# Optimization experiments

Hardware: AMD Instinct MI355X
Metric: run time of the kernel (lower is better)

Reference implementation:

```python
import jax, jax.numpy as jnp
import numpy as np

N_NODES = 100000
N_EDGES = 1000000
D = 64            # node_hidden
IN_DIM = 4 * D    # 256
MLP_H = 32
EPS = 1e-5


def setup_inputs() -> dict:
    key = jax.random.key(0)
    ks = jax.random.split(key, 6)
    h = jax.random.normal(ks[0], (N_NODES, D), dtype=jnp.float32)
    edge_pairs = jax.random.randint(ks[1], (2, N_EDGES), 0, N_NODES, dtype=jnp.int64)
    # LayerNorm params
    gamma = jnp.ones((IN_DIM,), dtype=jnp.float32)
    beta = jnp.zeros((IN_DIM,), dtype=jnp.float32)
    # MLP params (PyTorch Linear default init: U(-1/sqrt(fan_in), 1/sqrt(fan_in)))
    b1_bound = 1.0 / np.sqrt(IN_DIM)
    W1 = jax.random.uniform(ks[2], (IN_DIM, MLP_H), minval=-b1_bound, maxval=b1_bound, dtype=jnp.float32)
    b1 = jax.random.uniform(ks[3], (MLP_H,), minval=-b1_bound, maxval=b1_bound, dtype=jnp.float32)
    b2_bound = 1.0 / np.sqrt(MLP_H)
    W2 = jax.random.uniform(ks[4], (MLP_H, 1), minval=-b2_bound, maxval=b2_bound, dtype=jnp.float32)
    b2 = jax.random.uniform(ks[5], (1,), minval=-b2_bound, maxval=b2_bound, dtype=jnp.float32)
    return {"h": h, "edge_pairs": edge_pairs, "gamma": gamma, "beta": beta,
            "W1": W1, "b1": b1, "W2": W2, "b2": b2}


def reference(h, edge_pairs, gamma, beta, W1, b1, W2, b2):
    u = h[edge_pairs[0]]                                    # [E, D]
    v = h[edge_pairs[1]]                                    # [E, D]
    feat = jnp.concatenate([u, v, jnp.abs(u - v), u * v], axis=-1)  # [E, 4D]
    mu = jnp.mean(feat, axis=-1, keepdims=True)
    var = jnp.mean(jnp.square(feat - mu), axis=-1, keepdims=True)
    feat = (feat - mu) * jax.lax.rsqrt(var + EPS) * gamma + beta
    hmid = jax.nn.relu(feat @ W1 + b1)                      # [E, MLP_H]; dropout inactive at eval
    logit = hmid @ W2 + b2                                  # [E, 1]
    return logit.reshape(-1)
```

## Files before the change

kernel.cpp:

```cpp
#include <hip/hip_runtime.h>

#define N_EDGES 1000000
#define N_TILES (N_EDGES / 16)
#define N_NODES 100000

typedef __attribute__((ext_vector_type(8))) short short8;
typedef __attribute__((ext_vector_type(4))) float floatx4;

__device__ __forceinline__ short f2bf(float f) {
    __bf16 b = (__bf16)f;
    return __builtin_bit_cast(short, b);
}
__device__ __forceinline__ float bf2f(short s) {
    return (float)__builtin_bit_cast(__bf16, s);
}

__global__ __launch_bounds__(256) void conv_kernel(const float* __restrict__ h,
                                                   unsigned short* __restrict__ hb) {
    const int i = blockIdx.x * blockDim.x + threadIdx.x;
    if (i >= (N_NODES * 64) / 8) return;
    const float* p = h + (long)i * 8;
    floatx4 a = *(const floatx4*)p;
    floatx4 b = *(const floatx4*)(p + 4);
    short8 o;
    o[0] = f2bf(a[0]); o[1] = f2bf(a[1]); o[2] = f2bf(a[2]); o[3] = f2bf(a[3]);
    o[4] = f2bf(b[0]); o[5] = f2bf(b[1]); o[6] = f2bf(b[2]); o[7] = f2bf(b[3]);
    *(short8*)(hb + (long)i * 8) = o;
}

__global__ __launch_bounds__(256) void wprep_kernel(const float* __restrict__ gamma,
                                                    const float* __restrict__ beta,
                                                    const float* __restrict__ W1,
                                                    unsigned short* __restrict__ Wt,
                                                    float* __restrict__ GB) {
    const int n = blockIdx.x;
    const int k = threadIdx.x;
    const float w1 = W1[k * 32 + n];
    float G = gamma[k] * w1;
    float B = beta[k] * w1;
    Wt[n * 256 + k] = (unsigned short)f2bf(G);
    G += __shfl_xor(G, 1);  B += __shfl_xor(B, 1);
    G += __shfl_xor(G, 2);  B += __shfl_xor(B, 2);
    G += __shfl_xor(G, 4);  B += __shfl_xor(B, 4);
    G += __shfl_xor(G, 8);  B += __shfl_xor(B, 8);
    G += __shfl_xor(G, 16); B += __shfl_xor(B, 16);
    G += __shfl_xor(G, 32); B += __shfl_xor(B, 32);
    __shared__ float sG[4], sB[4];
    if ((k & 63) == 0) { sG[k >> 6] = G; sB[k >> 6] = B; }
    __syncthreads();
    if (k == 0) {
        GB[n]      = sG[0] + sG[1] + sG[2] + sG[3];
        GB[32 + n] = sB[0] + sB[1] + sB[2] + sB[3];
    }
}

__global__ __launch_bounds__(256) void edgehead_kernel(
    const unsigned short* __restrict__ hb,
    const int* __restrict__ ep,
    const float* __restrict__ b1,
    const float* __restrict__ W2,
    const float* __restrict__ b2p,
    const unsigned short* __restrict__ Wt,
    const float* __restrict__ GB,
    float* __restrict__ out)
{
    const int lane = threadIdx.x & 63;
    const int c = lane & 15;
    const int q = lane >> 4;
    const int wid = (int)((blockIdx.x * blockDim.x + threadIdx.x) >> 6);
    const int nw = (int)((gridDim.x * blockDim.x) >> 6);

    short8 bfrag[2][8];
#pragma unroll
    for (int nt = 0; nt < 2; ++nt)
#pragma unroll
        for (int s = 0; s < 8; ++s)
            bfrag[nt][s] = *(const short8*)(Wt + (nt * 16 + c) * 256 + 32 * s + 8 * q);

    const float Gn0 = GB[c],      Gn1 = GB[16 + c];
    const float Bn0 = GB[32 + c] + b1[c];
    const float Bn1 = GB[48 + c] + b1[16 + c];
    const float W20 = W2[c],      W21 = W2[16 + c];
    const float b2  = b2p[0];

    int t = wid;
    if (t >= N_TILES) return;
    int src = ep[t * 16 + c];
    int dst = ep[N_EDGES + t * 16 + c];

    for (; t < N_TILES; t += nw) {
        const unsigned short* pu = hb + (long)src * 64 + 8 * q;
        const unsigned short* pv = hb + (long)dst * 64 + 8 * q;
        short8 au0 = *(const short8*)(pu);
        short8 au1 = *(const short8*)(pu + 32);
        short8 av0 = *(const short8*)(pv);
        short8 av1 = *(const short8*)(pv + 32);

        {
            const int tn = t + nw;
            const int en = (tn < N_TILES ? tn : t) * 16 + c;
            src = ep[en];
            dst = ep[N_EDGES + en];
        }

        float fu0[8], fu1[8], fv0[8], fv1[8], fd0[8], fd1[8], fp0[8], fp1[8];
#pragma unroll
        for (int j = 0; j < 8; ++j) {
            fu0[j] = bf2f(au0[j]); fu1[j] = bf2f(au1[j]);
            fv0[j] = bf2f(av0[j]); fv1[j] = bf2f(av1[j]);
        }
#pragma unroll
        for (int j = 0; j < 8; ++j) {
            fd0[j] = fabsf(fu0[j] - fv0[j]);
            fd1[j] = fabsf(fu1[j] - fv1[j]);
            fp0[j] = fu0[j] * fv0[j];
            fp1[j] = fu1[j] * fv1[j];
        }
        short8 ad0, ad1, ap0, ap1;
#pragma unroll
        for (int j = 0; j < 8; ++j) {
            ad0[j] = f2bf(fd0[j]); ad1[j] = f2bf(fd1[j]);
            ap0[j] = f2bf(fp0[j]); ap1[j] = f2bf(fp1[j]);
        }

        float s1 = 0.f, s2 = 0.f;
#pragma unroll
        for (int j = 0; j < 8; ++j) {
            s1 += fu0[j] + fu1[j] + fv0[j] + fv1[j] + fd0[j] + fd1[j] + fp0[j] + fp1[j];
            s2 = fmaf(fu0[j], fu0[j], s2); s2 = fmaf(fu1[j], fu1[j], s2);
            s2 = fmaf(fv0[j], fv0[j], s2); s2 = fmaf(fv1[j], fv1[j], s2);
            s2 = fmaf(fd0[j], fd0[j], s2); s2 = fmaf(fd1[j], fd1[j], s2);
            s2 = fmaf(fp0[j], fp0[j], s2); s2 = fmaf(fp1[j], fp1[j], s2);
        }
        s1 += __shfl_xor(s1, 16); s2 += __shfl_xor(s2, 16);
        s1 += __shfl_xor(s1, 32); s2 += __shfl_xor(s2, 32);
        const float mu = s1 * (1.f / 256.f);
        const float var = fmaf(s2, 1.f / 256.f, -mu * mu);
        const float rs = rsqrtf(var + 1e-5f);

        floatx4 acc0 = {0.f, 0.f, 0.f, 0.f};
        floatx4 acc1 = {0.f, 0.f, 0.f, 0.f};
        acc0 = __builtin_amdgcn_mfma_f32_16x16x32_bf16(au0, bfrag[0][0], acc0, 0, 0, 0);
        acc1 = __builtin_amdgcn_mfma_f32_16x16x32_bf16(au0, bfrag[1][0], acc1, 0, 0, 0);
        acc0 = __builtin_amdgcn_mfma_f32_16x16x32_bf16(au1, bfrag[0][1], acc0, 0, 0, 0);
        acc1 = __builtin_amdgcn_mfma_f32_16x16x32_bf16(au1, bfrag[1][1], acc1, 0, 0, 0);
        acc0 = __builtin_amdgcn_mfma_f32_16x16x32_bf16(av0, bfrag[0][2], acc0, 0, 0, 0);
        acc1 = __builtin_amdgcn_mfma_f32_16x16x32_bf16(av0, bfrag[1][2], acc1, 0, 0, 0);
        acc0 = __builtin_amdgcn_mfma_f32_16x16x32_bf16(av1, bfrag[0][3], acc0, 0, 0, 0);
        acc1 = __builtin_amdgcn_mfma_f32_16x16x32_bf16(av1, bfrag[1][3], acc1, 0, 0, 0);
        acc0 = __builtin_amdgcn_mfma_f32_16x16x32_bf16(ad0, bfrag[0][4], acc0, 0, 0, 0);
        acc1 = __builtin_amdgcn_mfma_f32_16x16x32_bf16(ad0, bfrag[1][4], acc1, 0, 0, 0);
        acc0 = __builtin_amdgcn_mfma_f32_16x16x32_bf16(ad1, bfrag[0][5], acc0, 0, 0, 0);
        acc1 = __builtin_amdgcn_mfma_f32_16x16x32_bf16(ad1, bfrag[1][5], acc1, 0, 0, 0);
        acc0 = __builtin_amdgcn_mfma_f32_16x16x32_bf16(ap0, bfrag[0][6], acc0, 0, 0, 0);
        acc1 = __builtin_amdgcn_mfma_f32_16x16x32_bf16(ap0, bfrag[1][6], acc1, 0, 0, 0);
        acc0 = __builtin_amdgcn_mfma_f32_16x16x32_bf16(ap1, bfrag[0][7], acc0, 0, 0, 0);
        acc1 = __builtin_amdgcn_mfma_f32_16x16x32_bf16(ap1, bfrag[1][7], acc1, 0, 0, 0);

#pragma unroll
        for (int r = 0; r < 4; ++r) {
            const int srcl = 4 * q + r;
            const float mu_r = __shfl(mu, srcl);
            const float rs_r = __shfl(rs, srcl);
            float h0 = fmaf(rs_r, fmaf(-mu_r, Gn0, acc0[r]), Bn0); h0 = fmaxf(h0, 0.f);
            float h1 = fmaf(rs_r, fmaf(-mu_r, Gn1, acc1[r]), Bn1); h1 = fmaxf(h1, 0.f);
            float part = fmaf(h0, W20, h1 * W21);
            part += __shfl_xor(part, 1);
            part += __shfl_xor(part, 2);
            part += __shfl_xor(part, 4);
            part += __shfl_xor(part, 8);
            if (c == 0) out[t * 16 + 4 * q + r] = part + b2;
        }
    }
}

extern "C" void kernel_launch(void* const* d_in, const int* in_sizes, int n_in,
                              void* d_out, int out_size, void* d_ws, size_t ws_size,
                              hipStream_t stream) {
    const float* h     = (const float*)d_in[0];
    const int*   ep    = (const int*)d_in[1];
    const float* gamma = (const float*)d_in[2];
    const float* beta  = (const float*)d_in[3];
    const float* W1    = (const float*)d_in[4];
    const float* b1    = (const float*)d_in[5];
    const float* W2    = (const float*)d_in[6];
    const float* b2    = (const float*)d_in[7];
    float* out = (float*)d_out;

    unsigned short* hb = (unsigned short*)d_ws;
    unsigned short* Wt = (unsigned short*)((char*)d_ws + 12800000);
    float* GB = (float*)((char*)d_ws + 12800000 + 16384);

    conv_kernel<<<(N_NODES * 64 / 8 + 255) / 256, 256, 0, stream>>>(h, hb);
    wprep_kernel<<<32, 256, 0, stream>>>(gamma, beta, W1, Wt, GB);
    edgehead_kernel<<<2048, 256, 0, stream>>>(hb, ep, b1, W2, b2, Wt, GB, out);
}
```

Baseline: 153.6 us.

## Compute LayerNorm stats via MFMA and prefetch node rows one tile ahead

Computes the LayerNorm sum and sum of squares with extra MFMA instructions, one against an all-ones fragment and one as the Gram product of the feature fragment with itself, read from its diagonal. This replaces the per-lane VALU reductions and cross-lane shuffles. It also software-pipelines the gathered node rows one tile ahead and the edge indices two tiles ahead, to hide gather latency. The cost is double the MFMA count per tile, more live registers for the prefetched fragments, and statistics now taken from bf16-rounded features instead of fp32 values.

Result: faster. 145.7 us (-5.2%).

```diff
diff --git a/kernel.cpp b/kernel.cpp
--- a/kernel.cpp
+++ b/kernel.cpp
@@ -77,6 +77,10 @@
         for (int s = 0; s < 8; ++s)
             bfrag[nt][s] = *(const short8*)(Wt + (nt * 16 + c) * 256 + 32 * s + 8 * q);
 
+    short8 ones;
+#pragma unroll
+    for (int j = 0; j < 8; ++j) ones[j] = (short)0x3F80;
+
     const float Gn0 = GB[c],      Gn1 = GB[16 + c];
     const float Bn0 = GB[32 + c] + b1[c];
     const float Bn1 = GB[48 + c] + b1[16 + c];
@@ -85,83 +89,70 @@
 
     int t = wid;
     if (t >= N_TILES) return;
-    int src = ep[t * 16 + c];
-    int dst = ep[N_EDGES + t * 16 + c];
+
+    int s0 = ep[t * 16 + c];
+    int d0 = ep[N_EDGES + t * 16 + c];
+    short8 au0 = *(const short8*)(hb + (long)s0 * 64 + 8 * q);
+    short8 au1 = *(const short8*)(hb + (long)s0 * 64 + 8 * q + 32);
+    short8 av0 = *(const short8*)(hb + (long)d0 * 64 + 8 * q);
+    short8 av1 = *(const short8*)(hb + (long)d0 * 64 + 8 * q + 32);
+    int t1 = t + nw;
+    int e1 = (t1 < N_TILES ? t1 : t) * 16 + c;
+    int s1i = ep[e1];
+    int d1i = ep[N_EDGES + e1];
 
     for (; t < N_TILES; t += nw) {
-        const unsigned short* pu = hb + (long)src * 64 + 8 * q;
-        const unsigned short* pv = hb + (long)dst * 64 + 8 * q;
-        short8 au0 = *(const short8*)(pu);
-        short8 au1 = *(const short8*)(pu + 32);
-        short8 av0 = *(const short8*)(pv);
-        short8 av1 = *(const short8*)(pv + 32);
-
+        short8 nu0 = *(const short8*)(hb + (long)s1i * 64 + 8 * q);
+        short8 nu1 = *(const short8*)(hb + (long)s1i * 64 + 8 * q + 32);
+        short8 nv0 = *(const short8*)(hb + (long)d1i * 64 + 8 * q);
+        short8 nv1 = *(const short8*)(hb + (long)d1i * 64 + 8 * q + 32);
         {
-            const int tn = t + nw;
+            const int tn = t + 2 * nw;
             const int en = (tn < N_TILES ? tn : t) * 16 + c;
-            src = ep[en];
-            dst = ep[N_EDGES + en];
+            s1i = ep[en];
+            d1i = ep[N_EDGES + en];
         }
 
-        float fu0[8], fu1[8], fv0[8], fv1[8], fd0[8], fd1[8], fp0[8], fp1[8];
-#pragma unroll
-        for (int j = 0; j < 8; ++j) {
-            fu0[j] = bf2f(au0[j]); fu1[j] = bf2f(au1[j]);
-            fv0[j] = bf2f(av0[j]); fv1[j] = bf2f(av1[j]);
-        }
-#pragma unroll
-        for (int j = 0; j < 8; ++j) {
-            fd0[j] = fabsf(fu0[j] - fv0[j]);
-            fd1[j] = fabsf(fu1[j] - fv1[j]);
-            fp0[j] = fu0[j] * fv0[j];
-            fp1[j] = fu1[j] * fv1[j];
-        }
         short8 ad0, ad1, ap0, ap1;
 #pragma unroll
         for (int j = 0; j < 8; ++j) {
-            ad0[j] = f2bf(fd0[j]); ad1[j] = f2bf(fd1[j]);
-            ap0[j] = f2bf(fp0[j]); ap1[j] = f2bf(fp1[j]);
+            const float u0 = bf2f(au0[j]), u1 = bf2f(au1[j]);
+            const float v0 = bf2f(av0[j]), v1 = bf2f(av1[j]);
+            ad0[j] = f2bf(fabsf(u0 - v0));
+            ad1[j] = f2bf(fabsf(u1 - v1));
+            ap0[j] = f2bf(u0 * v0);
+            ap1[j] = f2bf(u1 * v1);
         }
-
-        float s1 = 0.f, s2 = 0.f;
-#pragma unroll
-        for (int j = 0; j < 8; ++j) {
-            s1 += fu0[j] + fu1[j] + fv0[j] + fv1[j] + fd0[j] + fd1[j] + fp0[j] + fp1[j];
-            s2 = fmaf(fu0[j], fu0[j], s2); s2 = fmaf(fu1[j], fu1[j], s2);
-            s2 = fmaf(fv0[j], fv0[j], s2); s2 = fmaf(fv1[j], fv1[j], s2);
-            s2 = fmaf(fd0[j], fd0[j], s2); s2 = fmaf(fd1[j], fd1[j], s2);
-            s2 = fmaf(fp0[j], fp0[j], s2); s2 = fmaf(fp1[j], fp1[j], s2);
-        }
-        s1 += __shfl_xor(s1, 16); s2 += __shfl_xor(s2, 16);
-        s1 += __shfl_xor(s1, 32); s2 += __shfl_xor(s2, 32);
-        const float mu = s1 * (1.f / 256.f);
-        const float var = fmaf(s2, 1.f / 256.f, -mu * mu);
-        const float rs = rsqrtf(var + 1e-5f);
 
         floatx4 acc0 = {0.f, 0.f, 0.f, 0.f};
         floatx4 acc1 = {0.f, 0.f, 0.f, 0.f};
-        acc0 = __builtin_amdgcn_mfma_f32_16x16x32_bf16(au0, bfrag[0][0], acc0, 0, 0, 0);
-        acc1 = __builtin_amdgcn_mfma_f32_16x16x32_bf16(au0, bfrag[1][0], acc1, 0, 0, 0);
-        acc0 = __builtin_amdgcn_mfma_f32_16x16x32_bf16(au1, bfrag[0][1], acc0, 0, 0, 0);
-        acc1 = __builtin_amdgcn_mfma_f32_16x16x32_bf16(au1, bfrag[1][1], acc1, 0, 0, 0);
-        acc0 = __builtin_amdgcn_mfma_f32_16x16x32_bf16(av0, bfrag[0][2], acc0, 0, 0, 0);
-        acc1 = __builtin_amdgcn_mfma_f32_16x16x32_bf16(av0, bfrag[1][2], acc1, 0, 0, 0);
-        acc0 = __builtin_amdgcn_mfma_f32_16x16x32_bf16(av1, bfrag[0][3], acc0, 0, 0, 0);
-        acc1 = __builtin_amdgcn_mfma_f32_16x16x32_bf16(av1, bfrag[1][3], acc1, 0, 0, 0);
-        acc0 = __builtin_amdgcn_mfma_f32_16x16x32_bf16(ad0, bfrag[0][4], acc0, 0, 0, 0);
-        acc1 = __builtin_amdgcn_mfma_f32_16x16x32_bf16(ad0, bfrag[1][4], acc1, 0, 0, 0);
-        acc0 = __builtin_amdgcn_mfma_f32_16x16x32_bf16(ad1, bfrag[0][5], acc0, 0, 0, 0);
-        acc1 = __builtin_amdgcn_mfma_f32_16x16x32_bf16(ad1, bfrag[1][5], acc1, 0, 0, 0);
-        acc0 = __builtin_amdgcn_mfma_f32_16x16x32_bf16(ap0, bfrag[0][6], acc0, 0, 0, 0);
-        acc1 = __builtin_amdgcn_mfma_f32_16x16x32_bf16(ap0, bfrag[1][6], acc1, 0, 0, 0);
-        acc0 = __builtin_amdgcn_mfma_f32_16x16x32_bf16(ap1, bfrag[0][7], acc0, 0, 0, 0);
-        acc1 = __builtin_amdgcn_mfma_f32_16x16x32_bf16(ap1, bfrag[1][7], acc1, 0, 0, 0);
+        floatx4 asum = {0.f, 0.f, 0.f, 0.f};
+        floatx4 agrm = {0.f, 0.f, 0.f, 0.f};
+#pragma unroll
+        for (int s = 0; s < 8; ++s) {
+            short8 af;
+            switch (s) {
+                case 0: af = au0; break;
+                case 1: af = au1; break;
+                case 2: af = av0; break;
+                case 3: af = av1; break;
+                case 4: af = ad0; break;
+                case 5: af = ad1; break;
+                case 6: af = ap0; break;
+                default: af = ap1; break;
+            }
+            acc0 = __builtin_amdgcn_mfma_f32_16x16x32_bf16(af, bfrag[0][s], acc0, 0, 0, 0);
+            acc1 = __builtin_amdgcn_mfma_f32_16x16x32_bf16(af, bfrag[1][s], acc1, 0, 0, 0);
+            asum = __builtin_amdgcn_mfma_f32_16x16x32_bf16(af, ones,       asum, 0, 0, 0);
+            agrm = __builtin_amdgcn_mfma_f32_16x16x32_bf16(af, af,         agrm, 0, 0, 0);
+        }
 
 #pragma unroll
         for (int r = 0; r < 4; ++r) {
-            const int srcl = 4 * q + r;
-            const float mu_r = __shfl(mu, srcl);
-            const float rs_r = __shfl(rs, srcl);
+            const float ss_r = __shfl(agrm[r], 20 * q + r);
+            const float mu_r = asum[r] * (1.f / 256.f);
+            const float var  = fmaf(ss_r, 1.f / 256.f, -mu_r * mu_r);
+            const float rs_r = rsqrtf(var + 1e-5f);
             float h0 = fmaf(rs_r, fmaf(-mu_r, Gn0, acc0[r]), Bn0); h0 = fmaxf(h0, 0.f);
             float h1 = fmaf(rs_r, fmaf(-mu_r, Gn1, acc1[r]), Bn1); h1 = fmaxf(h1, 0.f);
             float part = fmaf(h0, W20, h1 * W21);
@@ -171,6 +162,8 @@
             part += __shfl_xor(part, 8);
             if (c == 0) out[t * 16 + 4 * q + r] = part + b2;
         }
+
+        au0 = nu0; au1 = nu1; av0 = nv0; av1 = nv1;
     }
 }
 
```
